# Kernel optimization log

Measured on AMD Instinct MI355X. Metric: run time of the kernel, lower is better.

The kernel has to match this reference:

```python
import jax, jax.numpy as jnp
import numpy as np

K_BASE = 2048
K_MIN = 256
K_MAX = 4096
TEMPERATURE = 1.0
NEG_INF = float('-inf')


def setup_inputs() -> dict:
    key = jax.random.key(0)
    scores = jax.random.normal(key, (4, 2048, 8192), dtype=jnp.float32)
    return {"scores": scores, "seq_q": 2048, "seq_kv": 8192}


def _compute_adaptive_k(scores):
    # scores: [B, Sq, Skv]
    valid = scores != NEG_INF                          # [B, Sq, Skv]
    masked = jnp.where(valid, scores, 0.0)
    valid_counts = valid.sum(axis=-1).astype(scores.dtype)  # [B, Sq]
    # torch .var defaults to unbiased (ddof=1)
    score_var = jnp.var(masked, axis=-1, ddof=1)       # [B, Sq]
    var_norm = score_var / (score_var.mean() + 1e-8)
    k_scale = 1.0 / (1.0 + var_norm * TEMPERATURE)
    k_adaptive = K_BASE * (0.5 + k_scale)
    k_values = jnp.clip(k_adaptive, K_MIN, K_MAX)
    k_values = jnp.minimum(k_values, valid_counts)
    return k_values.astype(jnp.int32)                  # [B, Sq]


def reference(scores, seq_q, seq_kv):
    batch = scores.shape[0]
    k_values = _compute_adaptive_k(scores)             # [B, Sq]
    k_effective = min(K_MAX, seq_kv)                   # static int
    scores_for_topk = jnp.where(scores == NEG_INF, -1e9, scores)
    _, indices = jax.lax.top_k(scores_for_topk, k_effective)  # [B, Sq, k_eff]
    pos = jnp.arange(k_effective, dtype=jnp.int32)     # [k_eff]
    mask = pos[None, None, :] < k_values[:, :, None]   # [B, Sq, k_eff]
    gathered = jnp.take_along_axis(scores, indices, axis=-1)
    mask = mask & (gathered != NEG_INF)
    return indices, mask
```

## Files before the change

### kernel.cpp

```cpp
#include <hip/hip_runtime.h>
#include <math.h>

#define SEQ_KV 8192
#define KEFF   4096
#define THREADS 1024
#define NBIN   8192
#define SCAP   4608

typedef unsigned long long u64;
typedef unsigned int u32;

__device__ __forceinline__ int wave_incl_scan_i32(int x) {
  x += __builtin_amdgcn_update_dpp(0, x, 0x111, 0xF, 0xF, false);
  x += __builtin_amdgcn_update_dpp(0, x, 0x112, 0xF, 0xF, false);
  x += __builtin_amdgcn_update_dpp(0, x, 0x114, 0xF, 0xF, false);
  x += __builtin_amdgcn_update_dpp(0, x, 0x118, 0xF, 0xF, false);
  x += __builtin_amdgcn_update_dpp(0, x, 0x142, 0xA, 0xF, false);
  x += __builtin_amdgcn_update_dpp(0, x, 0x143, 0xC, 0xF, false);
  return x;
}
__device__ __forceinline__ float wave_incl_scan_f32(float x) {
#define STEPF(ctrl, rmask)                                                  \
  x += __int_as_float(__builtin_amdgcn_update_dpp(                          \
      0, __float_as_int(x), ctrl, rmask, 0xF, false));
  STEPF(0x111, 0xF) STEPF(0x112, 0xF) STEPF(0x114, 0xF) STEPF(0x118, 0xF)
  STEPF(0x142, 0xA) STEPF(0x143, 0xC)
#undef STEPF
  return x;
}

__device__ __forceinline__ int block_excl_scan(int v, int t, int* wsum) {
  const int lane = t & 63, w = t >> 6;
  int incl = wave_incl_scan_i32(v);
  if (lane == 63) wsum[w] = incl;
  __syncthreads();
  if (t == 0) {
    int run = 0;
#pragma unroll
    for (int i = 0; i < 16; ++i) { int c = wsum[i]; wsum[i] = run; run += c; }
  }
  __syncthreads();
  return (incl - v) + wsum[w];
}

__global__ __launch_bounds__(THREADS) void topk_kernel(
    const float* __restrict__ scores,
    float* __restrict__ var_out, int* __restrict__ cnt_out,
    int* __restrict__ out_idx) {
  __shared__ __align__(16) u32 hist[NBIN];
  __shared__ __align__(16) u64 S[SCAP];
  __shared__ float fsum[16], fsq[16];
  __shared__ int dcnt[16], wsum[16];

  const int t = threadIdx.x;
  const int row = blockIdx.x;
  const float* s = scores + (size_t)row * SEQ_KV;

  float4 f0 = *(const float4*)(s + 8 * t);
  float4 f1 = *(const float4*)(s + 8 * t + 4);
  float v[8] = {f0.x, f0.y, f0.z, f0.w, f1.x, f1.y, f1.z, f1.w};

  u64 r[8];
  int d[8];
  float sum = 0.0f, sq = 0.0f;
  int cnt = 0;
#pragma unroll
  for (int a = 0; a < 8; ++a) {
    u32 u = __float_as_uint(v[a]);
    u32 asc = ((int)u < 0) ? ~u : (u | 0x80000000u);
    r[a] = ((u64)(~asc) << 32) | (u32)(8 * t + a);
    float fd = fminf(fmaxf((4.0f - v[a]) * 1024.0f, 0.0f), 8191.0f);
    d[a] = (int)fd;
    bool val = (v[a] != -INFINITY);
    float m = val ? v[a] : 0.0f;
    sum += m;
    sq = fmaf(m, m, sq);
    cnt += val ? 1 : 0;
  }

  {
    uint4 z = {0u, 0u, 0u, 0u};
    *(uint4*)&hist[8 * t] = z;
    *(uint4*)&hist[8 * t + 4] = z;
  }

  sum = wave_incl_scan_f32(sum);
  sq = wave_incl_scan_f32(sq);
  cnt = wave_incl_scan_i32(cnt);
  if ((t & 63) == 63) { int w = t >> 6; fsum[w] = sum; fsq[w] = sq; dcnt[w] = cnt; }
  __syncthreads();

  int ord[8];
#pragma unroll
  for (int a = 0; a < 8; ++a) ord[a] = (int)atomicAdd(&hist[d[a]], 1u);

  if (t == 0) {
    float Ssum = 0.0f, Q = 0.0f; int C = 0;
#pragma unroll
    for (int w = 0; w < 16; ++w) { Ssum += fsum[w]; Q += fsq[w]; C += dcnt[w]; }
    const float N = (float)SEQ_KV;
    float mean = Ssum / N;
    float var = (Q - N * mean * mean) / (N - 1.0f);
    if (var < 0.0f) var = 0.0f;
    var_out[row] = var;
    cnt_out[row] = C;
  }
  __syncthreads();

  uint4 ca = *(uint4*)&hist[8 * t];
  uint4 cb = *(uint4*)&hist[8 * t + 4];
  int c[8] = {(int)ca.x, (int)ca.y, (int)ca.z, (int)ca.w,
              (int)cb.x, (int)cb.y, (int)cb.z, (int)cb.w};
  int tot = c[0] + c[1] + c[2] + c[3] + c[4] + c[5] + c[6] + c[7];
  int run = block_excl_scan(tot, t, wsum);
  {
    uint4 pa, pb;
    pa.x = (u32)run | ((u32)c[0] << 16); run += c[0];
    pa.y = (u32)run | ((u32)c[1] << 16); run += c[1];
    pa.z = (u32)run | ((u32)c[2] << 16); run += c[2];
    pa.w = (u32)run | ((u32)c[3] << 16); run += c[3];
    pb.x = (u32)run | ((u32)c[4] << 16); run += c[4];
    pb.y = (u32)run | ((u32)c[5] << 16); run += c[5];
    pb.z = (u32)run | ((u32)c[6] << 16); run += c[6];
    pb.w = (u32)run | ((u32)c[7] << 16); run += c[7];
    *(uint4*)&hist[8 * t] = pa;
    *(uint4*)&hist[8 * t + 4] = pb;
  }
  __syncthreads();

  u32 pc[8];
#pragma unroll
  for (int a = 0; a < 8; ++a) pc[a] = hist[d[a]];

#pragma unroll
  for (int a = 0; a < 8; ++a) {
    int st = (int)(pc[a] & 0xFFFFu);
    if (st < KEFF) {
      int pos = st + ord[a];
      if (pos < SCAP) S[pos] = r[a];
    }
  }
  __syncthreads();

  int* Sout = (int*)hist;
#pragma unroll
  for (int a = 0; a < 8; ++a) {
    int st = (int)(pc[a] & 0xFFFFu);
    if (st < KEFF) {
      int end = min(st + (int)(pc[a] >> 16), SCAP);
      const u64 k = r[a];
      int rr = st;
      for (int j = st; j < end; ++j) rr += (S[j] < k) ? 1 : 0;
      if (rr < KEFF) Sout[rr] = (int)(u32)k;
    }
  }
  __syncthreads();

  int4 o = *(int4*)&Sout[4 * t];
  *(int4*)(out_idx + (size_t)row * KEFF + 4 * t) = o;
}

__global__ __launch_bounds__(256) void mean_kernel(
    const float* __restrict__ var_in, float* __restrict__ mean_out, int rows) {
  float sum = 0.0f;
  for (int i = threadIdx.x; i < rows; i += 256) sum += var_in[i];
  sum = wave_incl_scan_f32(sum);
  __shared__ float part[4];
  const int w = threadIdx.x >> 6;
  if ((threadIdx.x & 63) == 63) part[w] = sum;
  __syncthreads();
  if (threadIdx.x == 0) {
    float tsum = part[0] + part[1] + part[2] + part[3];
    mean_out[0] = tsum / (float)rows;
  }
}

__global__ __launch_bounds__(256) void epilogue_kernel(
    const float* __restrict__ var_in, const float* __restrict__ mean_in,
    const int* __restrict__ cnt_in, int* __restrict__ out_mask) {
  const int row = blockIdx.x;
  const float vn = var_in[row] / (mean_in[0] + 1e-8f);
  float kad = 2048.0f * (0.5f + 1.0f / (1.0f + vn));
  kad = fminf(fmaxf(kad, 256.0f), 4096.0f);
  kad = fminf(kad, (float)cnt_in[row]);
  const int kv = (int)kad;

  int4* dst = (int4*)(out_mask + (size_t)row * KEFF);
  const int t = threadIdx.x;
#pragma unroll
  for (int c = 0; c < 4; ++c) {
    const int q = c * 256 + t;
    int4 mv;
    mv.x = (4 * q + 0 < kv) ? 1 : 0;
    mv.y = (4 * q + 1 < kv) ? 1 : 0;
    mv.z = (4 * q + 2 < kv) ? 1 : 0;
    mv.w = (4 * q + 3 < kv) ? 1 : 0;
    dst[q] = mv;
  }
}

extern "C" void kernel_launch(void* const* d_in, const int* in_sizes, int n_in,
                              void* d_out, int out_size, void* d_ws, size_t ws_size,
                              hipStream_t stream) {
  const float* scores = (const float*)d_in[0];
  const int rows = in_sizes[0] / SEQ_KV;

  float* var = (float*)d_ws;
  float* mean = var + rows;
  int* cnt = (int*)(mean + 1);

  int* out_idx = (int*)d_out;
  int* out_mask = out_idx + (size_t)rows * KEFF;

  topk_kernel<<<rows, THREADS, 0, stream>>>(scores, var, cnt, out_idx);
  mean_kernel<<<1, 256, 0, stream>>>(var, mean, rows);
  epilogue_kernel<<<rows, 256, 0, stream>>>(var, mean, cnt, out_mask);
}
```

Baseline: 197.7 us.

## Double histogram resolution with packed 16-bit bins and split key storage

Raises the bin count to 16384 and packs two 16-bit counters per 32-bit word, so each bin holds fewer elements and the quadratic within-bin ranking loop gets shorter. The 64-bit sort keys become a 32-bit value array plus a separate 16-bit index array, which lowers shared-memory traffic. Bins with a single element are no longer written to the staging buffer or ranked. In exchange the atomics and prefix scan must unpack the half-words, and each bin's count is now derived from the next bin's start.

```diff
diff --git a/kernel.cpp b/kernel.cpp
--- a/kernel.cpp
+++ b/kernel.cpp
@@ -4,11 +4,13 @@
 #define SEQ_KV 8192
 #define KEFF   4096
 #define THREADS 1024
-#define NBIN   8192
+#define NBIN   16384
+#define HWORDS (NBIN / 2)
 #define SCAP   4608
 
 typedef unsigned long long u64;
 typedef unsigned int u32;
+typedef unsigned short u16;
 
 __device__ __forceinline__ int wave_incl_scan_i32(int x) {
   x += __builtin_amdgcn_update_dpp(0, x, 0x111, 0xF, 0xF, false);
@@ -47,8 +49,9 @@
     const float* __restrict__ scores,
     float* __restrict__ var_out, int* __restrict__ cnt_out,
     int* __restrict__ out_idx) {
-  __shared__ __align__(16) u32 hist[NBIN];
-  __shared__ __align__(16) u64 S[SCAP];
+  __shared__ __align__(16) u32 hist[HWORDS + 1];
+  __shared__ __align__(16) u32 S32[SCAP];
+  __shared__ __align__(16) u16 S16[SCAP];
   __shared__ float fsum[16], fsq[16];
   __shared__ int dcnt[16], wsum[16];
 
@@ -60,16 +63,15 @@
   float4 f1 = *(const float4*)(s + 8 * t + 4);
   float v[8] = {f0.x, f0.y, f0.z, f0.w, f1.x, f1.y, f1.z, f1.w};
 
-  u64 r[8];
+  u32 asc[8];
   int d[8];
   float sum = 0.0f, sq = 0.0f;
   int cnt = 0;
 #pragma unroll
   for (int a = 0; a < 8; ++a) {
     u32 u = __float_as_uint(v[a]);
-    u32 asc = ((int)u < 0) ? ~u : (u | 0x80000000u);
-    r[a] = ((u64)(~asc) << 32) | (u32)(8 * t + a);
-    float fd = fminf(fmaxf((4.0f - v[a]) * 1024.0f, 0.0f), 8191.0f);
+    asc[a] = ((int)u < 0) ? ~u : (u | 0x80000000u);
+    float fd = fminf(fmaxf((4.0f - v[a]) * 2048.0f, 0.0f), 16383.0f);
     d[a] = (int)fd;
     bool val = (v[a] != -INFINITY);
     float m = val ? v[a] : 0.0f;
@@ -92,7 +94,11 @@
 
   int ord[8];
 #pragma unroll
-  for (int a = 0; a < 8; ++a) ord[a] = (int)atomicAdd(&hist[d[a]], 1u);
+  for (int a = 0; a < 8; ++a) {
+    int w = d[a] >> 1, sh = (d[a] & 1) << 4;
+    u32 old = atomicAdd(&hist[w], 1u << sh);
+    ord[a] = (int)((old >> sh) & 0xFFFFu);
+  }
 
   if (t == 0) {
     float Ssum = 0.0f, Q = 0.0f; int C = 0;
@@ -109,35 +115,45 @@
 
   uint4 ca = *(uint4*)&hist[8 * t];
   uint4 cb = *(uint4*)&hist[8 * t + 4];
-  int c[8] = {(int)ca.x, (int)ca.y, (int)ca.z, (int)ca.w,
-              (int)cb.x, (int)cb.y, (int)cb.z, (int)cb.w};
-  int tot = c[0] + c[1] + c[2] + c[3] + c[4] + c[5] + c[6] + c[7];
+  u32 cw[8] = {ca.x, ca.y, ca.z, ca.w, cb.x, cb.y, cb.z, cb.w};
+  int tot = 0;
+#pragma unroll
+  for (int i = 0; i < 8; ++i) tot += (int)(cw[i] & 0xFFFFu) + (int)(cw[i] >> 16);
   int run = block_excl_scan(tot, t, wsum);
   {
     uint4 pa, pb;
-    pa.x = (u32)run | ((u32)c[0] << 16); run += c[0];
-    pa.y = (u32)run | ((u32)c[1] << 16); run += c[1];
-    pa.z = (u32)run | ((u32)c[2] << 16); run += c[2];
-    pa.w = (u32)run | ((u32)c[3] << 16); run += c[3];
-    pb.x = (u32)run | ((u32)c[4] << 16); run += c[4];
-    pb.y = (u32)run | ((u32)c[5] << 16); run += c[5];
-    pb.z = (u32)run | ((u32)c[6] << 16); run += c[6];
-    pb.w = (u32)run | ((u32)c[7] << 16); run += c[7];
+    u32 pw[8];
+#pragma unroll
+    for (int i = 0; i < 8; ++i) {
+      u32 lo = (u32)run; run += (int)(cw[i] & 0xFFFFu);
+      u32 hi = (u32)run; run += (int)(cw[i] >> 16);
+      pw[i] = lo | (hi << 16);
+    }
+    pa.x = pw[0]; pa.y = pw[1]; pa.z = pw[2]; pa.w = pw[3];
+    pb.x = pw[4]; pb.y = pw[5]; pb.z = pw[6]; pb.w = pw[7];
     *(uint4*)&hist[8 * t] = pa;
     *(uint4*)&hist[8 * t + 4] = pb;
   }
-  __syncthreads();
-
-  u32 pc[8];
-#pragma unroll
-  for (int a = 0; a < 8; ++a) pc[a] = hist[d[a]];
-
-#pragma unroll
-  for (int a = 0; a < 8; ++a) {
-    int st = (int)(pc[a] & 0xFFFFu);
-    if (st < KEFF) {
-      int pos = st + ord[a];
-      if (pos < SCAP) S[pos] = r[a];
+  if (t == THREADS - 1) hist[HWORDS] = (u32)SEQ_KV;
+  __syncthreads();
+
+  int st[8], cn[8];
+#pragma unroll
+  for (int a = 0; a < 8; ++a) {
+    int w = d[a] >> 1;
+    u32 w0 = hist[w];
+    int s0, nx;
+    if (d[a] & 1) { s0 = (int)(w0 >> 16); nx = (int)(hist[w + 1] & 0xFFFFu); }
+    else          { s0 = (int)(w0 & 0xFFFFu); nx = (int)(w0 >> 16); }
+    st[a] = s0;
+    cn[a] = nx - s0;
+  }
+
+#pragma unroll
+  for (int a = 0; a < 8; ++a) {
+    if (st[a] < KEFF && cn[a] > 1) {
+      int pos = st[a] + ord[a];
+      if (pos < SCAP) { S32[pos] = asc[a]; S16[pos] = (u16)(8 * t + a); }
     }
   }
   __syncthreads();
@@ -145,13 +161,19 @@
   int* Sout = (int*)hist;
 #pragma unroll
   for (int a = 0; a < 8; ++a) {
-    int st = (int)(pc[a] & 0xFFFFu);
-    if (st < KEFF) {
-      int end = min(st + (int)(pc[a] >> 16), SCAP);
-      const u64 k = r[a];
-      int rr = st;
-      for (int j = st; j < end; ++j) rr += (S[j] < k) ? 1 : 0;
-      if (rr < KEFF) Sout[rr] = (int)(u32)k;
+    if (st[a] < KEFF) {
+      int rr = st[a];
+      if (cn[a] > 1) {
+        int end = min(st[a] + cn[a], SCAP);
+        const u32 me = asc[a];
+        const int mi = 8 * t + a;
+        for (int j = st[a]; j < end; ++j) {
+          u32 o = S32[j];
+          rr += (o > me) ? 1 : 0;
+          if (o == me) rr += (S16[j] < mi) ? 1 : 0;
+        }
+      }
+      if (rr < KEFF) Sout[rr] = 8 * t + a;
     }
   }
   __syncthreads();
```

After: 357.4 us. 80.8% more time.
